# Performance work log

Hardware: AMD Instinct MI355X
Metric: run time of the kernel (lower is better)

The kernel has to match this reference:

```python
import jax, jax.numpy as jnp
import numpy as np

B, L, D, H, T = 4, 1024, 1024, 16, 64


def cubic_interp_1d(vec, coords):
    # Catmull-Rom interpolation of 1D vec at real-valued coords (any shape).
    Lv = vec.shape[0]
    i = jnp.floor(coords).astype(jnp.int32)
    t = coords - i.astype(coords.dtype)
    im1 = jnp.clip(i - 1, 0, Lv - 1)
    i0 = jnp.clip(i, 0, Lv - 1)
    i1 = jnp.clip(i + 1, 0, Lv - 1)
    i2 = jnp.clip(i + 2, 0, Lv - 1)
    p0, p1, p2, p3 = vec[im1], vec[i0], vec[i1], vec[i2]
    t2 = t * t
    t3 = t2 * t
    return 0.5 * (2 * p1 + (-p0 + p2) * t + (2 * p0 - 5 * p1 + 4 * p2 - p3) * t2
                  + (-p0 + 3 * p1 - 3 * p2 + p3) * t3)


def linear_interp_1d(vec, coords):
    Lv = vec.shape[0]
    i = jnp.floor(coords).astype(jnp.int32)
    t = coords - i.astype(coords.dtype)
    i0 = jnp.clip(i, 0, Lv - 1)
    i1 = jnp.clip(i + 1, 0, Lv - 1)
    return vec[i0] * (1 - t) + vec[i1] * t


def setup_inputs() -> dict:
    key = jax.random.key(0)
    ks = jax.random.split(key, 12)
    s = 1.0 / np.sqrt(D)
    return {
        "x": jax.random.normal(ks[0], (B, L, D), jnp.float32),
        "t_enc": jax.random.normal(ks[1], (B, L, T), jnp.float32),
        "WQ": jax.random.normal(ks[2], (D, D), jnp.float32) * s,
        "WK": jax.random.normal(ks[3], (D, D), jnp.float32) * s,
        "WV": jax.random.normal(ks[4], (D, D), jnp.float32) * s,
        "WO": jax.random.normal(ks[5], (D, D), jnp.float32) * s,
        "bO": jnp.zeros((D,), jnp.float32),
        "Wt": jax.random.normal(ks[6], (T,), jnp.float32) * (1.0 / np.sqrt(T)),
        "bt": jnp.zeros((), jnp.float32),
        "p_mat": jax.random.normal(ks[7], (D, L), jnp.float32) * 0.02,
        "r_mat": jax.random.normal(ks[8], (D, L), jnp.float32) * 0.02,
        "alpha": jnp.ones((H,), jnp.float32),
        "beta": jnp.ones((H,), jnp.float32),
        "gamma": jnp.zeros((H,), jnp.float32),
    }


def reference(x, t_enc, WQ, WK, WV, WO, bO, Wt, bt, p_mat, r_mat, alpha, beta, gamma):
    Bx, Lx, Dx = x.shape
    d = Dx // H
    # projections: torch Linear y = x @ W.T
    Q = (x @ WQ.T).reshape(Bx, Lx, H, d).transpose(0, 2, 1, 3)  # [B,H,L,d]
    K = (x @ WK.T).reshape(Bx, Lx, H, d).transpose(0, 2, 1, 3)
    V = (x @ WV.T).reshape(Bx, Lx, H, d).transpose(0, 2, 1, 3)
    P = x.reshape(Bx, Lx, H, d).transpose(0, 2, 1, 3)
    # time-warped coordinates
    tau = jax.nn.sigmoid(t_enc @ Wt + bt)          # [B,L]
    coords = tau * (Lx - 1)
    # q_sca = cubic_interp(p_mat, coords).sum(-1); interp is linear in p_mat,
    # so interpolate the d-summed vector (same math, no [B,L,d] blowup).
    q_sca = cubic_interp_1d(p_mat.sum(0), coords)  # [B,L]
    delta = jnp.abs(coords[:, :, None] - coords[:, None, :])   # [B,L,L]
    r_sca = linear_interp_1d(r_mat.sum(0), delta)              # [B,L,L]
    qsum = q_sca[:, :, None] + q_sca[:, None, :]               # [B,L,L]
    Pij = jnp.einsum('bhid,bhjd->bhij', P, P)                  # [B,H,L,L]
    a = alpha[None, :, None, None]
    b = beta[None, :, None, None]
    c = gamma[None, :, None, None]
    S = a * qsum[:, None] + b * r_sca[:, None] + c
    scores = jnp.einsum('bhid,bhjd->bhij', Q, K) / jnp.sqrt(jnp.asarray(d, x.dtype)) + S * Pij
    attn = jax.nn.softmax(scores, axis=-1)
    out = jnp.einsum('bhij,bhjd->bhid', attn, V)
    out = out.transpose(0, 2, 1, 3).reshape(Bx, Lx, Dx)
    return out @ WO.T + bO
```

## Files before the change

### kernel.cpp

```cpp
#include <hip/hip_runtime.h>
#include <cstdint>
#include <cstddef>

typedef __attribute__((ext_vector_type(8))) short s8v;
typedef __attribute__((ext_vector_type(4))) float f32x4;

__device__ __forceinline__ unsigned short f2bf(float f) {
  unsigned int u = __builtin_bit_cast(unsigned int, f);
  unsigned int r = (u + 0x7fffu + ((u >> 16) & 1u)) >> 16;
  return (unsigned short)r;
}
__device__ __forceinline__ float bf2f(unsigned short s) {
  unsigned int u = ((unsigned int)s) << 16;
  return __builtin_bit_cast(float, u);
}

__device__ __forceinline__ void gload16(const void* g, void* l) {
  __builtin_amdgcn_global_load_lds(
      (const __attribute__((address_space(1))) void*)g,
      (__attribute__((address_space(3))) void*)l, 16, 0, 0);
}


__global__ __launch_bounds__(256)
void colsum_kernel(const float* __restrict__ p_mat, const float* __restrict__ r_mat,
                   float* __restrict__ q_vec, float* __restrict__ r_vec) {
  int col = blockIdx.x * 256 + threadIdx.x;
  int d0 = blockIdx.y * 32;
  float sp = 0.f, sr = 0.f;
  for (int d = d0; d < d0 + 32; ++d) {
    sp += p_mat[d * 1024 + col];
    sr += r_mat[d * 1024 + col];
  }
  atomicAdd(&q_vec[col], sp);
  atomicAdd(&r_vec[col], sr);
}

__global__ __launch_bounds__(256)
void coords_kernel(const float* __restrict__ t_enc, const float* __restrict__ Wt,
                   const float* __restrict__ bt, const float* __restrict__ q_vec,
                   float* __restrict__ coords, float* __restrict__ q_sca) {
  int item = blockIdx.x * 4 + (threadIdx.x >> 6);
  int lane = threadIdx.x & 63;
  float v = t_enc[(size_t)item * 64 + lane] * Wt[lane];
  v += __shfl_xor(v, 32);
  v += __shfl_xor(v, 16);
  v += __shfl_xor(v, 8);
  v += __shfl_xor(v, 4);
  v += __shfl_xor(v, 2);
  v += __shfl_xor(v, 1);
  if (lane == 0) {
    float z = v + bt[0];
    float tau = 1.0f / (1.0f + expf(-z));
    float c = tau * 1023.0f;
    coords[item] = c;
    float fi = floorf(c);
    int i = (int)fi;
    float t = c - fi;
    int im1 = i - 1; if (im1 < 0) im1 = 0; if (im1 > 1023) im1 = 1023;
    int i0 = i; if (i0 < 0) i0 = 0; if (i0 > 1023) i0 = 1023;
    int i1 = i + 1; if (i1 > 1023) i1 = 1023;
    int i2 = i + 2; if (i2 > 1023) i2 = 1023;
    float p0 = q_vec[im1], p1 = q_vec[i0], p2 = q_vec[i1], p3 = q_vec[i2];
    float t2 = t * t, t3 = t2 * t;
    q_sca[item] = 0.5f * (2.f * p1 + (-p0 + p2) * t +
                          (2.f * p0 - 5.f * p1 + 4.f * p2 - p3) * t2 +
                          (-p0 + 3.f * p1 - 3.f * p2 + p3) * t3);
  }
}

__global__ __launch_bounds__(256)
void conv_all_kernel(const float* __restrict__ x,
                     const float* __restrict__ w0, const float* __restrict__ w1,
                     const float* __restrict__ w2, const float* __restrict__ w3,
                     unsigned short* __restrict__ xb, unsigned short* __restrict__ xlo,
                     unsigned short* __restrict__ wb) {
  int bx = blockIdx.x;
  if (bx < 16384) {
    int i = bx * 256 + threadIdx.x;
    float f = x[i];
    unsigned short h = f2bf(f);
    xb[i] = h;
    xlo[i] = f2bf(f - bf2f(h));
  } else {
    int i = (bx - 16384) * 256 + threadIdx.x;
    int sel = i >> 20;
    const float* w = (sel == 0) ? w0 : (sel == 1) ? w1 : (sel == 2) ? w2 : w3;
    wb[i] = f2bf(w[i & 0xFFFFF]);
  }
}


__global__ __launch_bounds__(256, 2)
void gemm_qkv_kernel(const unsigned short* __restrict__ Abuf,
                     const unsigned short* __restrict__ Wb,
                     unsigned short* __restrict__ Qb,
                     unsigned short* __restrict__ Kb,
                     unsigned short* __restrict__ Vb) {
  __shared__ unsigned short As[2][128 * 64];
  __shared__ unsigned short Bs[2][128 * 64];
  const int tid = threadIdx.x, w = tid >> 6, l = tid & 63;
  const int sel = blockIdx.x >> 3;
  const int nb = (blockIdx.x & 7) * 128;
  const int m0 = blockIdx.y * 128;
  const unsigned short* Bbuf = Wb + ((size_t)sel << 20);
  const int wr = w >> 1, wc = w & 1;
  const int ll = l & 15, lg = l >> 4;
  const int cs = (((l & 7) ^ ((l >> 3) & 7)) * 8);

  const f32x4 zero4 = {0.f, 0.f, 0.f, 0.f};
  f32x4 acc[4][4];
  #pragma unroll
  for (int i = 0; i < 4; ++i) {
    #pragma unroll
    for (int j = 0; j < 4; ++j) acc[i][j] = zero4;
  }

  auto stage = [&](int kt, int buf) {
    #pragma unroll
    for (int q = 0; q < 4; ++q) {
      const int seg = w * 4 + q;
      const int row = seg * 8 + (l >> 3);
      const int col = kt * 64 + cs;
      gload16(Abuf + (size_t)(m0 + row) * 1024 + col, &As[buf][seg * 512 + l * 8]);
      gload16(Bbuf + (size_t)(nb + row) * 1024 + col, &Bs[buf][seg * 512 + l * 8]);
    }
  };

  stage(0, 0);
  for (int kt = 0; kt < 16; ++kt) {
    __syncthreads();
    if (kt < 15) stage(kt + 1, (kt + 1) & 1);
    const int bb = kt & 1;
    #pragma unroll
    for (int ks = 0; ks < 2; ++ks) {
      const int gsw = ((ks * 4 + lg) ^ (ll & 7)) * 8;
      s8v af[4], bf[4];
      #pragma unroll
      for (int mi = 0; mi < 4; ++mi)
        af[mi] = *(const s8v*)&As[bb][(wr * 64 + mi * 16 + ll) * 64 + gsw];
      #pragma unroll
      for (int ni = 0; ni < 4; ++ni)
        bf[ni] = *(const s8v*)&Bs[bb][(wc * 64 + ni * 16 + ll) * 64 + gsw];
      #pragma unroll
      for (int mi = 0; mi < 4; ++mi) {
        #pragma unroll
        for (int ni = 0; ni < 4; ++ni)
          acc[mi][ni] = __builtin_amdgcn_mfma_f32_16x16x32_bf16(af[mi], bf[ni], acc[mi][ni], 0, 0, 0);
      }
    }
  }

  unsigned short* dst = (sel == 0) ? Qb : ((sel == 1) ? Kb : Vb);
  unsigned short* ch = &As[0][0];
  const int err = tid >> 3;
  const int ecb = tid & 7;
  #pragma unroll
  for (int mi = 0; mi < 4; ++mi) {
    __syncthreads();
    #pragma unroll
    for (int ni = 0; ni < 4; ++ni) {
      #pragma unroll
      for (int r = 0; r < 4; ++r)
        ch[(wr * 16 + lg * 4 + r) * 136 + wc * 64 + ni * 16 + ll] = f2bf(acc[mi][ni][r]);
    }
    __syncthreads();
    int m = m0 + (err >> 4) * 64 + mi * 16 + (err & 15);
    int ncol = nb + ecb * 16;
    int bb2 = m >> 10, lr = m & 1023, hh = ncol >> 6, dd = ncol & 63;
    unsigned short* gp = &dst[(((size_t)bb2 * 16 + hh) * 1024 + lr) * 64 + dd];
    *(s8v*)(gp)     = *(const s8v*)&ch[err * 136 + ecb * 16];
    *(s8v*)(gp + 8) = *(const s8v*)&ch[err * 136 + ecb * 16 + 8];
  }
}


__global__ __launch_bounds__(256, 2)
void gemm_out_kernel(const unsigned short* __restrict__ Abuf,
                     const unsigned short* __restrict__ Bbuf,
                     const float* __restrict__ bO,
                     float* __restrict__ out) {
  __shared__ unsigned short As[2][128 * 64];
  __shared__ unsigned short Bs[2][128 * 64];
  const int tid = threadIdx.x, w = tid >> 6, l = tid & 63;
  const int nb = blockIdx.x * 128;
  const int m0 = blockIdx.y * 128;
  const int wr = w >> 1, wc = w & 1;
  const int ll = l & 15, lg = l >> 4;
  const int cs = (((l & 7) ^ ((l >> 3) & 7)) * 8);

  const f32x4 zero4 = {0.f, 0.f, 0.f, 0.f};
  f32x4 acc[4][4];
  #pragma unroll
  for (int i = 0; i < 4; ++i) {
    #pragma unroll
    for (int j = 0; j < 4; ++j) acc[i][j] = zero4;
  }

  auto stage = [&](int kt, int buf) {
    #pragma unroll
    for (int q = 0; q < 4; ++q) {
      const int seg = w * 4 + q;
      const int row = seg * 8 + (l >> 3);
      const int col = kt * 64 + cs;
      gload16(Abuf + (size_t)(m0 + row) * 1024 + col, &As[buf][seg * 512 + l * 8]);
      gload16(Bbuf + (size_t)(nb + row) * 1024 + col, &Bs[buf][seg * 512 + l * 8]);
    }
  };

  stage(0, 0);
  for (int kt = 0; kt < 16; ++kt) {
    __syncthreads();
    if (kt < 15) stage(kt + 1, (kt + 1) & 1);
    const int bb = kt & 1;
    #pragma unroll
    for (int ks = 0; ks < 2; ++ks) {
      const int gsw = ((ks * 4 + lg) ^ (ll & 7)) * 8;
      s8v af[4], bf[4];
      #pragma unroll
      for (int mi = 0; mi < 4; ++mi)
        af[mi] = *(const s8v*)&As[bb][(wr * 64 + mi * 16 + ll) * 64 + gsw];
      #pragma unroll
      for (int ni = 0; ni < 4; ++ni)
        bf[ni] = *(const s8v*)&Bs[bb][(wc * 64 + ni * 16 + ll) * 64 + gsw];
      #pragma unroll
      for (int mi = 0; mi < 4; ++mi) {
        #pragma unroll
        for (int ni = 0; ni < 4; ++ni)
          acc[mi][ni] = __builtin_amdgcn_mfma_f32_16x16x32_bf16(af[mi], bf[ni], acc[mi][ni], 0, 0, 0);
      }
    }
  }

  #pragma unroll
  for (int mi = 0; mi < 4; ++mi) {
    #pragma unroll
    for (int ni = 0; ni < 4; ++ni) {
      #pragma unroll
      for (int r = 0; r < 4; ++r) {
        int m = m0 + wr * 64 + mi * 16 + (l >> 4) * 4 + r;
        int ncol = nb + wc * 64 + ni * 16 + ll;
        out[(size_t)m * 1024 + ncol] = acc[mi][ni][r] + bO[ncol];
      }
    }
  }
}


__global__ __launch_bounds__(512, 2)
void attn_kernel(const unsigned short* __restrict__ Qb,
                 const unsigned short* __restrict__ Kb,
                 const unsigned short* __restrict__ Vb,
                 const unsigned short* __restrict__ xb,
                 const unsigned short* __restrict__ xlo,
                 const float* __restrict__ coords,
                 const float* __restrict__ q_sca,
                 const float* __restrict__ r_vec,
                 const float* __restrict__ alpha,
                 const float* __restrict__ beta,
                 const float* __restrict__ gamma,
                 unsigned short* __restrict__ AO) {
  __shared__ float r_s[1026];
  __shared__ unsigned short Ks[2][64 * 64];
  __shared__ unsigned short Ph[2][64 * 64];
  __shared__ unsigned short Pl[2][64 * 64];
  __shared__ unsigned short Vt[64 * 72];
  __shared__ unsigned short pbuf[8][16 * 72];

  const int tid = threadIdx.x;
  const int w = tid >> 6;
  const int l = tid & 63;
  const int gid = blockIdx.x;
  const int bh = (gid & 7) * 8 + ((gid >> 3) >> 3);
  const int xt = (gid >> 3) & 7;
  const int b = bh >> 4;
  const int h = bh & 15;
  const int iw = xt * 128 + w * 16;

  for (int t = tid; t < 1024; t += 512) r_s[t] = r_vec[t];
  if (tid < 2) r_s[1024 + tid] = r_vec[1023];

  const float INVLN2 = 1.4426950408889634f;
  const float a_h = alpha[h] * INVLN2, b_h = beta[h] * INVLN2, c_h = gamma[h] * INVLN2;
  const int lg = l >> 4;
  const int ll = l & 15;
  const int rowg = lg * 4;
  const int akg = lg * 8;

  float aqi[4], ci[4];
  #pragma unroll
  for (int r = 0; r < 4; ++r) {
    aqi[r] = fmaf(a_h, q_sca[b * 1024 + iw + rowg + r], c_h);
    ci[r] = coords[b * 1024 + iw + rowg + r];
  }

  s8v qf[2], pih[2], pil[2];
  {
    const unsigned short* qp = Qb + ((size_t)bh * 1024 + iw + ll) * 64 + akg;
    qf[0] = *(const s8v*)(qp);
    qf[1] = *(const s8v*)(qp + 32);
    const unsigned short* xp = xb + ((size_t)b * 1024 + iw + ll) * 1024 + h * 64 + akg;
    pih[0] = *(const s8v*)(xp);
    pih[1] = *(const s8v*)(xp + 32);
    const unsigned short* xq = xlo + ((size_t)b * 1024 + iw + ll) * 1024 + h * 64 + akg;
    pil[0] = *(const s8v*)(xq);
    pil[1] = *(const s8v*)(xq + 32);
  }

  const f32x4 zero4 = {0.f, 0.f, 0.f, 0.f};
  f32x4 o[4];
  #pragma unroll
  for (int ds = 0; ds < 4; ++ds) o[ds] = zero4;
  float mrow[4], lsum[4];
  #pragma unroll
  for (int r = 0; r < 4; ++r) { mrow[r] = -3.0e38f; lsum[r] = 0.f; }

  unsigned short* pw = pbuf[w];
  const int cs = (((l & 7) ^ ((l >> 3) & 7)) * 8);
  const int srow = l >> 3;

  auto stage = [&](int j0, int buf) {
    const int row = w * 8 + srow;
    gload16(Kb + ((size_t)bh * 1024 + j0 + row) * 64 + cs, &Ks[buf][w * 512 + l * 8]);
    gload16(xb + ((size_t)b * 1024 + j0 + row) * 1024 + h * 64 + cs, &Ph[buf][w * 512 + l * 8]);
    gload16(xlo + ((size_t)b * 1024 + j0 + row) * 1024 + h * 64 + cs, &Pl[buf][w * 512 + l * 8]);
  };
  auto vload = [&](int j0) -> s8v {
    return *(const s8v*)(Vb + ((size_t)bh * 1024 + j0 + l) * 64 + w * 8);
  };
  auto vwrite = [&](const s8v& vv) {
    #pragma unroll
    for (int e = 0; e < 8; ++e) Vt[(w * 8 + e) * 72 + l] = (unsigned short)vv[e];
  };

  stage(0, 0);
  s8v vv0 = vload(0);
  stage(64, 1);
  s8v vv1 = vload(64);
  vwrite(vv0);
  __syncthreads();

#define ATTN_TILE(T, PAR, VCONS, VPROD)                                          \
  {                                                                              \
    const int j0 = (T) * 64;                                                     \
    float cj[4], aqj[4];                                                         \
    _Pragma("unroll")                                                            \
    for (int s = 0; s < 4; ++s) {                                                \
      cj[s] = coords[b * 1024 + j0 + ll + 16 * s];                               \
      aqj[s] = a_h * q_sca[b * 1024 + j0 + ll + 16 * s];                         \
    }                                                                            \
    f32x4 aqk[4], app[4];                                                        \
    _Pragma("unroll")                                                            \
    for (int s = 0; s < 4; ++s) { aqk[s] = zero4; app[s] = zero4; }              \
    _Pragma("unroll")                                                            \
    for (int ks = 0; ks < 2; ++ks) {                                             \
      _Pragma("unroll")                                                          \
      for (int s = 0; s < 4; ++s) {                                              \
        const int rb = (ll + 16 * s) * 64 + (((ks * 4 + lg) ^ (ll & 7)) * 8);    \
        s8v kf = *(const s8v*)&Ks[PAR][rb];                                      \
        s8v hf = *(const s8v*)&Ph[PAR][rb];                                      \
        s8v lf = *(const s8v*)&Pl[PAR][rb];                                      \
        aqk[s] = __builtin_amdgcn_mfma_f32_16x16x32_bf16(qf[ks], kf, aqk[s], 0, 0, 0);   \
        app[s] = __builtin_amdgcn_mfma_f32_16x16x32_bf16(pih[ks], hf, app[s], 0, 0, 0);  \
        app[s] = __builtin_amdgcn_mfma_f32_16x16x32_bf16(pih[ks], lf, app[s], 0, 0, 0);  \
        app[s] = __builtin_amdgcn_mfma_f32_16x16x32_bf16(pil[ks], hf, app[s], 0, 0, 0);  \
      }                                                                          \
    }                                                                            \
    float tmax[4];                                                               \
    _Pragma("unroll")                                                            \
    for (int r = 0; r < 4; ++r) tmax[r] = -3.0e38f;                              \
    _Pragma("unroll")                                                            \
    for (int s = 0; s < 4; ++s) {                                                \
      _Pragma("unroll")                                                          \
      for (int r = 0; r < 4; ++r) {                                              \
        float delta = fabsf(ci[r] - cj[s]);                                      \
        int i0 = (int)delta;                                                     \
        float tt = delta - (float)i0;                                            \
        float r0 = r_s[i0];                                                      \
        float r1 = r_s[i0 + 1];                                                  \
        float rs = fmaf(tt, r1 - r0, r0);                                        \
        float S = fmaf(b_h, rs, aqi[r] + aqj[s]);                                \
        float v = fmaf(0.18033688f, aqk[s][r], S * app[s][r]);                   \
        app[s][r] = v;                                                           \
        tmax[r] = fmaxf(tmax[r], v);                                             \
      }                                                                          \
    }                                                                            \
    _Pragma("unroll")                                                            \
    for (int r = 0; r < 4; ++r) {                                                \
      float v = tmax[r];                                                         \
      v = fmaxf(v, __shfl_xor(v, 1));                                            \
      v = fmaxf(v, __shfl_xor(v, 2));                                            \
      v = fmaxf(v, __shfl_xor(v, 4));                                            \
      v = fmaxf(v, __shfl_xor(v, 8));                                            \
      float mn = fmaxf(mrow[r], v);                                              \
      float scale = exp2f(mrow[r] - mn);                                         \
      mrow[r] = mn;                                                              \
      lsum[r] *= scale;                                                          \
      o[0][r] *= scale; o[1][r] *= scale; o[2][r] *= scale; o[3][r] *= scale;    \
    }                                                                            \
    _Pragma("unroll")                                                            \
    for (int s = 0; s < 4; ++s) {                                                \
      _Pragma("unroll")                                                          \
      for (int r = 0; r < 4; ++r) {                                              \
        float e = exp2f(app[s][r] - mrow[r]);                                    \
        lsum[r] += e;                                                            \
        pw[(rowg + r) * 72 + ll + 16 * s] = f2bf(e);                             \
      }                                                                          \
    }                                                                            \
    _Pragma("unroll")                                                            \
    for (int ks = 0; ks < 2; ++ks) {                                             \
      s8v pa = *(const s8v*)&pw[ll * 72 + ks * 32 + akg];                        \
      _Pragma("unroll")                                                          \
      for (int dq = 0; dq < 4; ++dq) {                                           \
        s8v vf = *(const s8v*)&Vt[(ll + 16 * dq) * 72 + ks * 32 + akg];          \
        o[dq] = __builtin_amdgcn_mfma_f32_16x16x32_bf16(pa, vf, o[dq], 0, 0, 0); \
      }                                                                          \
    }                                                                            \
    __syncthreads();                          \
    if ((T) < 15) {                                                              \
      vwrite(VCONS);                                           \
      if ((T) < 14) {                                                            \
        stage((T) + 2 > 15 ? 0 : ((T) + 2) * 64, PAR);                           \
        VPROD = vload(((T) + 2) * 64);                                           \
      }                                                                          \
      asm volatile("s_waitcnt lgkmcnt(0)" ::: "memory");                         \
      __builtin_amdgcn_sched_barrier(0);                                         \
      __builtin_amdgcn_s_barrier();                                              \
    }                                                                            \
  }

  for (int t2 = 0; t2 < 16; t2 += 2) {
    ATTN_TILE(t2, 0, vv1, vv0);
    ATTN_TILE(t2 + 1, 1, vv0, vv1);
  }
#undef ATTN_TILE

  #pragma unroll
  for (int r = 0; r < 4; ++r) {
    float v = lsum[r];
    v += __shfl_xor(v, 1);
    v += __shfl_xor(v, 2);
    v += __shfl_xor(v, 4);
    v += __shfl_xor(v, 8);
    lsum[r] = 1.0f / v;
  }
  #pragma unroll
  for (int ds = 0; ds < 4; ++ds) {
    #pragma unroll
    for (int r = 0; r < 4; ++r) {
      AO[((size_t)b * 1024 + iw + rowg + r) * 1024 + h * 64 + ll + 16 * ds] =
          f2bf(o[ds][r] * lsum[r]);
    }
  }
}


extern "C" void kernel_launch(void* const* d_in, const int* in_sizes, int n_in,
                              void* d_out, int out_size, void* d_ws, size_t ws_size,
                              hipStream_t stream) {
  const float* x     = (const float*)d_in[0];
  const float* t_enc = (const float*)d_in[1];
  const float* WQ    = (const float*)d_in[2];
  const float* WK    = (const float*)d_in[3];
  const float* WV    = (const float*)d_in[4];
  const float* WO    = (const float*)d_in[5];
  const float* bO    = (const float*)d_in[6];
  const float* Wt    = (const float*)d_in[7];
  const float* bt    = (const float*)d_in[8];
  const float* p_mat = (const float*)d_in[9];
  const float* r_mat = (const float*)d_in[10];
  const float* alpha = (const float*)d_in[11];
  const float* beta  = (const float*)d_in[12];
  const float* gamma = (const float*)d_in[13];
  float* out = (float*)d_out;

  char* ws = (char*)d_ws;
  unsigned short* xb  = (unsigned short*)(ws + ((size_t)0 << 20));
  unsigned short* xlo = (unsigned short*)(ws + ((size_t)8 << 20));
  unsigned short* wb  = (unsigned short*)(ws + ((size_t)16 << 20));
  unsigned short* Qb  = (unsigned short*)(ws + ((size_t)24 << 20));
  unsigned short* Kb  = (unsigned short*)(ws + ((size_t)32 << 20));
  unsigned short* Vb  = (unsigned short*)(ws + ((size_t)40 << 20));
  unsigned short* AO  = (unsigned short*)(ws + ((size_t)48 << 20));
  float* q_vec  = (float*)(ws + ((size_t)56 << 20));
  float* r_vec  = q_vec + 1024;
  float* coords = r_vec + 1024;
  float* q_sca  = coords + 4096;

  hipMemsetAsync(q_vec, 0, 2048 * sizeof(float), stream);
  colsum_kernel<<<dim3(4, 32), 256, 0, stream>>>(p_mat, r_mat, q_vec, r_vec);
  coords_kernel<<<1024, 256, 0, stream>>>(t_enc, Wt, bt, q_vec, coords, q_sca);
  conv_all_kernel<<<32768, 256, 0, stream>>>(x, WQ, WK, WV, WO, xb, xlo, wb);
  gemm_qkv_kernel<<<dim3(24, 32), 256, 0, stream>>>(xb, wb, Qb, Kb, Vb);
  attn_kernel<<<512, 512, 0, stream>>>(Qb, Kb, Vb, xb, xlo, coords, q_sca,
                                       r_vec, alpha, beta, gamma, AO);
  gemm_out_kernel<<<dim3(8, 32), 256, 0, stream>>>(AO, wb + ((size_t)3 << 20), bO, out);
}
```

Baseline: 284.0 us.

## Vectorize conversion kernel, swizzle attention LDS, pair r lookups, truncate P to bf16

```diff
diff --git a/kernel.cpp b/kernel.cpp
--- a/kernel.cpp
+++ b/kernel.cpp
@@ -76,17 +76,32 @@
                      unsigned short* __restrict__ xb, unsigned short* __restrict__ xlo,
                      unsigned short* __restrict__ wb) {
   int bx = blockIdx.x;
-  if (bx < 16384) {
-    int i = bx * 256 + threadIdx.x;
-    float f = x[i];
-    unsigned short h = f2bf(f);
-    xb[i] = h;
-    xlo[i] = f2bf(f - bf2f(h));
+  if (bx < 2048) {
+    size_t i8 = ((size_t)bx * 256 + threadIdx.x) * 8;
+    float4 a = *(const float4*)(x + i8);
+    float4 b = *(const float4*)(x + i8 + 4);
+    float v[8] = {a.x, a.y, a.z, a.w, b.x, b.y, b.z, b.w};
+    s8v h, lo;
+    #pragma unroll
+    for (int j = 0; j < 8; ++j) {
+      unsigned short hh = f2bf(v[j]);
+      h[j] = (short)hh;
+      lo[j] = (short)f2bf(v[j] - bf2f(hh));
+    }
+    *(s8v*)(xb + i8) = h;
+    *(s8v*)(xlo + i8) = lo;
   } else {
-    int i = (bx - 16384) * 256 + threadIdx.x;
-    int sel = i >> 20;
+    size_t i8 = ((size_t)(bx - 2048) * 256 + threadIdx.x) * 8;
+    int sel = (int)(i8 >> 20);
     const float* w = (sel == 0) ? w0 : (sel == 1) ? w1 : (sel == 2) ? w2 : w3;
-    wb[i] = f2bf(w[i & 0xFFFFF]);
+    size_t off = i8 & 0xFFFFF;
+    float4 a = *(const float4*)(w + off);
+    float4 b = *(const float4*)(w + off + 4);
+    float v[8] = {a.x, a.y, a.z, a.w, b.x, b.y, b.z, b.w};
+    s8v h;
+    #pragma unroll
+    for (int j = 0; j < 8; ++j) h[j] = (short)f2bf(v[j]);
+    *(s8v*)(wb + i8) = h;
   }
 }
 
@@ -260,12 +275,12 @@
                  const float* __restrict__ beta,
                  const float* __restrict__ gamma,
                  unsigned short* __restrict__ AO) {
-  __shared__ float r_s[1026];
+  __shared__ float2 rp_s[1024];
   __shared__ unsigned short Ks[2][64 * 64];
   __shared__ unsigned short Ph[2][64 * 64];
   __shared__ unsigned short Pl[2][64 * 64];
-  __shared__ unsigned short Vt[64 * 72];
-  __shared__ unsigned short pbuf[8][16 * 72];
+  __shared__ unsigned short Vt[64 * 64];
+  __shared__ unsigned short pbuf[8][16 * 64];
 
   const int tid = threadIdx.x;
   const int w = tid >> 6;
@@ -277,8 +292,11 @@
   const int h = bh & 15;
   const int iw = xt * 128 + w * 16;
 
-  for (int t = tid; t < 1024; t += 512) r_s[t] = r_vec[t];
-  if (tid < 2) r_s[1024 + tid] = r_vec[1023];
+  for (int t = tid; t < 1024; t += 512) {
+    float r0 = r_vec[t];
+    float r1 = r_vec[t < 1023 ? t + 1 : 1023];
+    rp_s[t] = make_float2(r0, r1);
+  }
 
   const float INVLN2 = 1.4426950408889634f;
   const float a_h = alpha[h] * INVLN2, b_h = beta[h] * INVLN2, c_h = gamma[h] * INVLN2;
@@ -330,7 +348,10 @@
   };
   auto vwrite = [&](const s8v& vv) {
     #pragma unroll
-    for (int e = 0; e < 8; ++e) Vt[(w * 8 + e) * 72 + l] = (unsigned short)vv[e];
+    for (int e = 0; e < 8; ++e) {
+      const int row = w * 8 + e;
+      Vt[row * 64 + (((l >> 3) ^ (row & 7)) * 8) + (l & 7)] = (unsigned short)vv[e];
+    }
   };
 
   stage(0, 0);
@@ -376,9 +397,8 @@
         float delta = fabsf(ci[r] - cj[s]);                                      \
         int i0 = (int)delta;                                                     \
         float tt = delta - (float)i0;                                            \
-        float r0 = r_s[i0];                                                      \
-        float r1 = r_s[i0 + 1];                                                  \
-        float rs = fmaf(tt, r1 - r0, r0);                                        \
+        float2 rr = rp_s[i0];                                                    \
+        float rs = fmaf(tt, rr.y - rr.x, rr.x);                                  \
         float S = fmaf(b_h, rs, aqi[r] + aqj[s]);                                \
         float v = fmaf(0.18033688f, aqk[s][r], S * app[s][r]);                   \
         app[s][r] = v;                                                           \
@@ -400,19 +420,23 @@
     }                                                                            \
     _Pragma("unroll")                                                            \
     for (int s = 0; s < 4; ++s) {                                                \
+      const int pg = ((2 * s + (ll >> 3)));                                      \
       _Pragma("unroll")                                                          \
       for (int r = 0; r < 4; ++r) {                                              \
         float e = exp2f(app[s][r] - mrow[r]);                                    \
         lsum[r] += e;                                                            \
-        pw[(rowg + r) * 72 + ll + 16 * s] = f2bf(e);                             \
+        const int row = rowg + r;                                                \
+        pw[row * 64 + ((pg ^ (row & 7)) * 8) + (ll & 7)] =                       \
+            (unsigned short)(__builtin_bit_cast(unsigned int, e) >> 16);         \
       }                                                                          \
     }                                                                            \
     _Pragma("unroll")                                                            \
     for (int ks = 0; ks < 2; ++ks) {                                             \
-      s8v pa = *(const s8v*)&pw[ll * 72 + ks * 32 + akg];                        \
+      s8v pa = *(const s8v*)&pw[ll * 64 + (((ks * 4 + lg) ^ (ll & 7)) * 8)];     \
       _Pragma("unroll")                                                          \
       for (int dq = 0; dq < 4; ++dq) {                                           \
-        s8v vf = *(const s8v*)&Vt[(ll + 16 * dq) * 72 + ks * 32 + akg];          \
+        const int vrow = ll + 16 * dq;                                           \
+        s8v vf = *(const s8v*)&Vt[vrow * 64 + (((ks * 4 + lg) ^ (ll & 7)) * 8)]; \
         o[dq] = __builtin_amdgcn_mfma_f32_16x16x32_bf16(pa, vf, o[dq], 0, 0, 0); \
       }                                                                          \
     }                                                                            \
@@ -490,7 +514,7 @@
   hipMemsetAsync(q_vec, 0, 2048 * sizeof(float), stream);
   colsum_kernel<<<dim3(4, 32), 256, 0, stream>>>(p_mat, r_mat, q_vec, r_vec);
   coords_kernel<<<1024, 256, 0, stream>>>(t_enc, Wt, bt, q_vec, coords, q_sca);
-  conv_all_kernel<<<32768, 256, 0, stream>>>(x, WQ, WK, WV, WO, xb, xlo, wb);
+  conv_all_kernel<<<4096, 256, 0, stream>>>(x, WQ, WK, WV, WO, xb, xlo, wb);
   gemm_qkv_kernel<<<dim3(24, 32), 256, 0, stream>>>(xb, wb, Qb, Kb, Vb);
   attn_kernel<<<512, 512, 0, stream>>>(Qb, Kb, Vb, xb, xlo, coords, q_sca,
                                        r_vec, alpha, beta, gamma, AO);
```

New measurement: 267.7 us. -5.7%, faster.
